# Optimization experiments

Hardware: AMD Instinct MI355X
Metric: run time of the kernel (lower is better)

## Reference

```python
import jax, jax.numpy as jnp
import numpy as np

B, LI, LT, DM, H = 1, 2048, 384, 2560, 20
DH = DM // H  # 128
EPS = 1e-05


def _rms(x, w):
    # torch.nn.RMSNorm over last dim (inner_dim), elementwise affine w
    return x * jax.lax.rsqrt(jnp.mean(x * x, axis=-1, keepdims=True) + EPS) * w


def _apply_rope(x, rope):
    # x: [B, L, H, D]; rope: [1, L, 1, D/2, 2, 2] (flux-style freqs_cis)
    xr = x.reshape(x.shape[0], x.shape[1], x.shape[2], -1, 1, 2)  # [B,L,H,D/2,1,2]
    out = rope[..., 0] * xr[..., 0] + rope[..., 1] * xr[..., 1]   # [B,L,H,D/2,2]
    return out.reshape(x.shape)


def _sdpa(q, k, v):
    # q,k,v: [B, L, H, D] -> out [B, L, H*D]; scale 1/sqrt(D)
    scale = 1.0 / np.sqrt(q.shape[-1]).astype(np.float32)
    scores = jnp.einsum('bqhd,bkhd->bhqk', q, k) * scale
    p = jax.nn.softmax(scores, axis=-1)
    o = jnp.einsum('bhqk,bkhd->bqhd', p, v)
    return o.reshape(o.shape[0], o.shape[1], -1)


def _lin(x, W, b):
    return x @ W.T + b


def _forward(img, txt, rope, img_masks,
             Wq, bq, Wk, bk, Wv, bv, Wo, bo, qn, kn,
             Wq_t, bq_t, Wk_t, bk_t, Wv_t, bv_t, Wo_t, bo_t, qn_t, kn_t):
    bsz = img.shape[0]
    # img stream: proj -> RMSNorm -> head split
    iq = _rms(_lin(img, Wq, bq), qn).reshape(bsz, -1, H, DH)
    ik = _rms(_lin(img, Wk, bk), kn).reshape(bsz, -1, H, DH)
    iv = _lin(img, Wv, bv).reshape(bsz, -1, H, DH)
    ik = ik * img_masks[:, :, None, None]
    # txt stream
    tq = _rms(_lin(txt, Wq_t, bq_t), qn_t).reshape(bsz, -1, H, DH)
    tk = _rms(_lin(txt, Wk_t, bk_t), kn_t).reshape(bsz, -1, H, DH)
    tv = _lin(txt, Wv_t, bv_t).reshape(bsz, -1, H, DH)
    # concat streams, apply rope, attention
    q = jnp.concatenate([iq, tq], axis=1)
    k = jnp.concatenate([ik, tk], axis=1)
    v = jnp.concatenate([iv, tv], axis=1)
    q = _apply_rope(q, rope)
    k = _apply_rope(k, rope)
    attn = _sdpa(q, k, v)  # [B, LI+LT, DM]
    img_attn, txt_attn = attn[:, :LI], attn[:, LI:]
    return _lin(img_attn, Wo, bo), _lin(txt_attn, Wo_t, bo_t)


def setup_inputs() -> dict:
    key = jax.random.key(0)
    ks = jax.random.split(key, 16)
    s = 0.02
    inp = {
        'img': jax.random.normal(ks[0], (B, LI, DM), jnp.float32),
        'txt': jax.random.normal(ks[1], (B, LT, DM), jnp.float32),
        'rope': jax.random.normal(ks[2], (1, LI + LT, 1, DH // 2, 2, 2), jnp.float32),
        'img_masks': jnp.ones((B, LI), jnp.float32),
    }
    wnames = ['Wq', 'Wk', 'Wv', 'Wo', 'Wq_t', 'Wk_t', 'Wv_t', 'Wo_t']
    for i, n in enumerate(wnames):
        inp[n] = jax.random.normal(ks[3 + i], (DM, DM), jnp.float32) * s
        inp['b' + n[1:]] = jnp.zeros((DM,), jnp.float32)
    for i, n in enumerate(['qn', 'kn', 'qn_t', 'kn_t']):
        inp[n] = jax.random.uniform(ks[11 + i], (DM,), jnp.float32, 0.5, 1.5)
    return inp


def reference(img, txt, rope, img_masks,
              Wq, bq, Wk, bk, Wv, bv, Wo, bo, qn, kn,
              Wq_t, bq_t, Wk_t, bk_t, Wv_t, bv_t, Wo_t, bo_t, qn_t, kn_t):
    return _forward(img, txt, rope, img_masks,
                    Wq, bq, Wk, bk, Wv, bv, Wo, bo, qn, kn,
                    Wq_t, bq_t, Wk_t, bk_t, Wv_t, bv_t, Wo_t, bo_t, qn_t, kn_t)
```

## Files before the change

### kernel.cpp

```cpp
#include <hip/hip_runtime.h>
#include <math.h>

#define LI 2048
#define LT 384
#define LSEQ 2432
#define DM 2560
#define NH 20
#define DH 128
#define SCALE 0.08838834764831845f

typedef __bf16 bf16x8 __attribute__((ext_vector_type(8)));
typedef __bf16 bf16x4 __attribute__((ext_vector_type(4)));
typedef __bf16 bf16x2 __attribute__((ext_vector_type(2)));
typedef float f32x4 __attribute__((ext_vector_type(4)));

__device__ __forceinline__ void async_copy16(const void* gsrc, void* lds_uniform) {
    __builtin_amdgcn_global_load_lds(
        (const __attribute__((address_space(1))) unsigned int*)gsrc,
        (__attribute__((address_space(3))) unsigned int*)lds_uniform,
        16, 0, 0);
}


__global__ __launch_bounds__(256) void cvt8_kernel(
    const float* __restrict__ s0, const float* __restrict__ s1,
    const float* __restrict__ s2, const float* __restrict__ s3,
    const float* __restrict__ s4, const float* __restrict__ s5,
    const float* __restrict__ s6, const float* __restrict__ s7,
    __bf16* __restrict__ dst)
{
    const float* srcs[8] = {s0, s1, s2, s3, s4, s5, s6, s7};
    const float* s = srcs[blockIdx.y];
    __bf16* d = dst + (size_t)blockIdx.y * (size_t)DM * DM;
    int i = blockIdx.x * 256 + threadIdx.x;
    const float4* sp = (const float4*)s + (size_t)i * 2;
    float4 a = sp[0], b = sp[1];
    bf16x8 o = {(__bf16)a.x, (__bf16)a.y, (__bf16)a.z, (__bf16)a.w,
                (__bf16)b.x, (__bf16)b.y, (__bf16)b.z, (__bf16)b.w};
    *((bf16x8*)d + i) = o;
}

__global__ __launch_bounds__(256) void cvt_kernel(
    const float* __restrict__ s, __bf16* __restrict__ d, int n8)
{
    int i = blockIdx.x * 256 + threadIdx.x;
    if (i >= n8) return;
    const float4* sp = (const float4*)s + (size_t)i * 2;
    float4 a = sp[0], b = sp[1];
    bf16x8 o = {(__bf16)a.x, (__bf16)a.y, (__bf16)a.z, (__bf16)a.w,
                (__bf16)b.x, (__bf16)b.y, (__bf16)b.z, (__bf16)b.w};
    *((bf16x8*)d + i) = o;
}


__device__ __forceinline__ void gemm_core(
    const __bf16* __restrict__ Ab,
    const __bf16* __restrict__ Bb,
    const float* __restrict__ bias,
    float* __restrict__ Cb,
    __bf16* sA, __bf16* sB)
{
    const int t = threadIdx.x, wave = t >> 6, lane = t & 63;
    const int l15 = lane & 15, quad = lane >> 4;
    const int wm = wave >> 1, wn = wave & 1;

    f32x4 acc[4][4];
#pragma unroll
    for (int i = 0; i < 4; i++)
#pragma unroll
        for (int j = 0; j < 4; j++) acc[i][j] = f32x4{0.f, 0.f, 0.f, 0.f};

    size_t soff[4];
#pragma unroll
    for (int j = 0; j < 4; j++) {
        int c = j * 256 + t;
        int row = c >> 3, u = c & 7;
        soff[j] = (size_t)row * DM + ((u ^ (row & 7)) * 8);
    }

    for (int k0 = 0; k0 < DM; k0 += 64) {
        __syncthreads();
#pragma unroll
        for (int j = 0; j < 4; j++)
            async_copy16(Ab + soff[j] + k0, (char*)sA + (j * 256 + wave * 64) * 16);
#pragma unroll
        for (int j = 0; j < 4; j++)
            async_copy16(Bb + soff[j] + k0, (char*)sB + (j * 256 + wave * 64) * 16);
        __syncthreads();

#pragma unroll
        for (int ks = 0; ks < 2; ks++) {
            bf16x8 af[4], bg[4];
#pragma unroll
            for (int mt = 0; mt < 4; mt++) {
                int r = wm * 64 + mt * 16 + l15;
                af[mt] = *(const bf16x8*)(sA + r * 64 + (((quad + ks * 4) ^ (r & 7)) * 8));
            }
#pragma unroll
            for (int nt = 0; nt < 4; nt++) {
                int r = wn * 64 + nt * 16 + l15;
                bg[nt] = *(const bf16x8*)(sB + r * 64 + (((quad + ks * 4) ^ (r & 7)) * 8));
            }
#pragma unroll
            for (int mt = 0; mt < 4; mt++)
#pragma unroll
                for (int nt = 0; nt < 4; nt++)
                    acc[mt][nt] = __builtin_amdgcn_mfma_f32_16x16x32_bf16(af[mt], bg[nt], acc[mt][nt], 0, 0, 0);
        }
    }

#pragma unroll
    for (int mt = 0; mt < 4; mt++) {
        const int row = wm * 64 + mt * 16 + quad * 4;
#pragma unroll
        for (int nt = 0; nt < 4; nt++) {
            const int col = wn * 64 + nt * 16 + l15;
            const float bv = bias[col];
            float* cp = Cb + (size_t)row * DM + col;
            cp[0]        = acc[mt][nt][0] + bv;
            cp[DM]       = acc[mt][nt][1] + bv;
            cp[2 * DM]   = acc[mt][nt][2] + bv;
            cp[3 * DM]   = acc[mt][nt][3] + bv;
        }
    }
}

__device__ __forceinline__ void qkv_body(
    int nblk, int mblk,
    const __bf16* __restrict__ xbf, const __bf16* __restrict__ wbf,
    const float* __restrict__ bq, const float* __restrict__ bk, const float* __restrict__ bv,
    const float* __restrict__ bq_t, const float* __restrict__ bk_t, const float* __restrict__ bv_t,
    float* __restrict__ qraw, float* __restrict__ kraw, float* __restrict__ vraw,
    __bf16* sA, __bf16* sB)
{
    const int which = nblk / 20;
    const int nloc = (nblk % 20) * 128;
    const bool is_txt = (mblk >= 16);
    const size_t WELEM = (size_t)DM * DM;
    const int widx = which + (is_txt ? 4 : 0);
    const __bf16* W = wbf + (size_t)widx * WELEM;
    const float* bias = (which == 0) ? (is_txt ? bq_t : bq)
                      : (which == 1) ? (is_txt ? bk_t : bk)
                                     : (is_txt ? bv_t : bv);
    float* C = (which == 0) ? qraw : (which == 1) ? kraw : vraw;
    gemm_core(xbf + (size_t)mblk * 128 * DM, W + (size_t)nloc * DM, bias + nloc,
              C + (size_t)mblk * 128 * DM + nloc, sA, sB);
}

__global__ __launch_bounds__(256, 4) void gemm_qkv_a_kernel(
    const __bf16* __restrict__ xbf, const __bf16* __restrict__ wbf,
    const float* __restrict__ bq, const float* __restrict__ bk, const float* __restrict__ bv,
    const float* __restrict__ bq_t, const float* __restrict__ bk_t, const float* __restrict__ bv_t,
    float* __restrict__ qraw, float* __restrict__ kraw, float* __restrict__ vraw)
{
    __shared__ alignas(16) __bf16 sA[128 * 64];
    __shared__ alignas(16) __bf16 sB[128 * 64];
    qkv_body(blockIdx.x, blockIdx.y, xbf, wbf, bq, bk, bv, bq_t, bk_t, bv_t,
             qraw, kraw, vraw, sA, sB);
}

__global__ __launch_bounds__(256, 4) void gemm_qkv_b_kernel(
    const __bf16* __restrict__ xbf, const __bf16* __restrict__ wbf,
    const float* __restrict__ bq, const float* __restrict__ bk, const float* __restrict__ bv,
    const float* __restrict__ bq_t, const float* __restrict__ bk_t, const float* __restrict__ bv_t,
    float* __restrict__ qraw, float* __restrict__ kraw, float* __restrict__ vraw)
{
    __shared__ alignas(16) __bf16 sA[128 * 64];
    __shared__ alignas(16) __bf16 sB[128 * 64];
    qkv_body(blockIdx.x, blockIdx.y + 10, xbf, wbf, bq, bk, bv, bq_t, bk_t, bv_t,
             qraw, kraw, vraw, sA, sB);
}

__global__ __launch_bounds__(256, 4) void gemm_out_kernel(
    const __bf16* __restrict__ attnbf, const __bf16* __restrict__ wbf,
    const float* __restrict__ bo, const float* __restrict__ bo_t,
    float* __restrict__ out)
{
    __shared__ alignas(16) __bf16 sA[128 * 64];
    __shared__ alignas(16) __bf16 sB[128 * 64];
    const int nblk = blockIdx.x, mblk = blockIdx.y;
    const bool is_txt = (mblk >= 16);
    const size_t WELEM = (size_t)DM * DM;
    const __bf16* W = wbf + (size_t)(is_txt ? 7 : 3) * WELEM;
    const float* bias = (is_txt ? bo_t : bo) + nblk * 128;
    gemm_core(attnbf + (size_t)mblk * 128 * DM, W + (size_t)nblk * 128 * DM, bias,
              out + (size_t)mblk * 128 * DM + nblk * 128, sA, sB);
}


__global__ __launch_bounds__(256) void rmsrope_kernel(
    const float* __restrict__ qraw, const float* __restrict__ kraw,
    const float* __restrict__ rope, const float* __restrict__ img_masks,
    const float* __restrict__ qn, const float* __restrict__ kn,
    const float* __restrict__ qn_t, const float* __restrict__ kn_t,
    __bf16* __restrict__ qbf, __bf16* __restrict__ kbf)
{
    const int l = blockIdx.x, t = threadIdx.x;
    const int wave = t >> 6, lane = t & 63;
    const bool is_img = (l < LI);
    const float* qw = is_img ? qn : qn_t;
    const float* kw = is_img ? kn : kn_t;
    const float kmask = is_img ? img_masks[l] : 1.0f;
    const float* qr = qraw + (size_t)l * DM;
    const float* kr = kraw + (size_t)l * DM;

    float2 qv[5], kv[5];
    float sq = 0.f, sk = 0.f;
#pragma unroll
    for (int j = 0; j < 5; j++) {
        int c2 = j * 256 + t;
        qv[j] = *(const float2*)(qr + 2 * c2);
        kv[j] = *(const float2*)(kr + 2 * c2);
        sq += qv[j].x * qv[j].x + qv[j].y * qv[j].y;
        sk += kv[j].x * kv[j].x + kv[j].y * kv[j].y;
    }
#pragma unroll
    for (int m = 32; m; m >>= 1) { sq += __shfl_xor(sq, m); sk += __shfl_xor(sk, m); }
    __shared__ float redq[4], redk[4];
    if (lane == 0) { redq[wave] = sq; redk[wave] = sk; }
    __syncthreads();
    sq = redq[0] + redq[1] + redq[2] + redq[3];
    sk = redk[0] + redk[1] + redk[2] + redk[3];
    const float rq = rsqrtf(sq * (1.0f / DM) + 1e-5f);
    const float rk = rsqrtf(sk * (1.0f / DM) + 1e-5f) * kmask;

#pragma unroll
    for (int j = 0; j < 5; j++) {
        int c2 = j * 256 + t;
        int c = 2 * c2;
        float4 rp = *(const float4*)(rope + ((size_t)l * 64 + (c2 & 63)) * 4);
        float2 w2q = *(const float2*)(qw + c);
        float2 w2k = *(const float2*)(kw + c);
        float x0 = qv[j].x * rq * w2q.x, x1 = qv[j].y * rq * w2q.y;
        bf16x2 oq = {(__bf16)(rp.x * x0 + rp.y * x1), (__bf16)(rp.z * x0 + rp.w * x1)};
        *(bf16x2*)(qbf + (size_t)l * DM + c) = oq;
        float y0 = kv[j].x * rk * w2k.x, y1 = kv[j].y * rk * w2k.y;
        bf16x2 ok = {(__bf16)(rp.x * y0 + rp.y * y1), (__bf16)(rp.z * y0 + rp.w * y1)};
        *(bf16x2*)(kbf + (size_t)l * DM + c) = ok;
    }
}


__global__ __launch_bounds__(256) void transpose_cvt_kernel(
    const float* __restrict__ src, __bf16* __restrict__ dst)
{
    __shared__ float tile[32][33];
    const int c0 = blockIdx.x * 32;
    const int r0 = blockIdx.y * 32;
    const int tc = threadIdx.x & 31, tr = threadIdx.x >> 5;
#pragma unroll
    for (int j = 0; j < 4; j++)
        tile[tr + j * 8][tc] = src[(size_t)(r0 + tr + j * 8) * DM + c0 + tc];
    __syncthreads();
#pragma unroll
    for (int j = 0; j < 4; j++)
        dst[(size_t)(c0 + tr + j * 8) * LSEQ + r0 + tc] = (__bf16)tile[tc][tr + j * 8];
}


__global__ __launch_bounds__(256, 4) void flash_kernel(
    const __bf16* __restrict__ qb, const __bf16* __restrict__ kb,
    const __bf16* __restrict__ vt, __bf16* __restrict__ ob)
{
    __shared__ alignas(16) __bf16 sK[64 * DH];
    __shared__ alignas(16) __bf16 sV[DH * 64];
    __shared__ alignas(16) __bf16 sP[4 * 16 * 64];
    const int head = blockIdx.x;
    const int q0 = blockIdx.y * 64;
    const int t = threadIdx.x, wave = t >> 6, lane = t & 63;
    const int l15 = lane & 15, quad = lane >> 4;
    const int qrow = q0 + wave * 16 + l15;

    bf16x8 aq[4];
#pragma unroll
    for (int d = 0; d < 4; d++)
        aq[d] = *(const bf16x8*)(qb + (size_t)qrow * DM + head * DH + d * 32 + quad * 8);

    int koff[4], voff[4];
#pragma unroll
    for (int j = 0; j < 4; j++) {
        int ck = (wave * 4 + j) * 64 + lane;
        int krow = ck >> 4, ku = (ck & 15) ^ (krow & 7);
        koff[j] = krow * DM + head * DH + ku * 8;
        int cv = (wave * 4 + j) * 64 + lane;
        int vrow = cv >> 3, vu = (cv & 7) ^ (vrow & 7);
        voff[j] = (head * DH + vrow) * LSEQ + vu * 8;
    }
    char* const dK = (char*)sK + wave * 4096 + lane * 16;
    char* const dV = (char*)sV + wave * 4096 + lane * 16;

    f32x4 o[8];
#pragma unroll
    for (int i = 0; i < 8; i++) o[i] = f32x4{0.f, 0.f, 0.f, 0.f};
    float m_i = -INFINITY, l_i = 0.f;
    __bf16* pw = sP + wave * (16 * 64);

    bf16x8 rk[4], rv[4];
#pragma unroll
    for (int j = 0; j < 4; j++) {
        rk[j] = *(const bf16x8*)(kb + koff[j]);
        rv[j] = *(const bf16x8*)(vt + voff[j]);
    }

    for (int kv0 = 0; kv0 < LSEQ; kv0 += 64) {
        __syncthreads();
#pragma unroll
        for (int j = 0; j < 4; j++) {
            *(bf16x8*)(dK + j * 1024) = rk[j];
            *(bf16x8*)(dV + j * 1024) = rv[j];
        }
        __syncthreads();

        if (kv0 + 64 < LSEQ) {
#pragma unroll
            for (int j = 0; j < 4; j++) {
                rk[j] = *(const bf16x8*)(kb + koff[j] + (size_t)(kv0 + 64) * DM);
                rv[j] = *(const bf16x8*)(vt + voff[j] + (kv0 + 64));
            }
        }

        f32x4 st[4];
        __builtin_amdgcn_s_setprio(1);
#pragma unroll
        for (int b = 0; b < 4; b++) {
            st[b] = f32x4{0.f, 0.f, 0.f, 0.f};
#pragma unroll
            for (int d = 0; d < 4; d++) {
                int row = b * 16 + l15;
                bf16x8 ak = *(const bf16x8*)(sK + row * 128 + (((d * 4 + quad) ^ (row & 7)) * 8));
                st[b] = __builtin_amdgcn_mfma_f32_16x16x32_bf16(ak, aq[d], st[b], 0, 0, 0);
            }
        }
        __builtin_amdgcn_s_setprio(0);

        float mx = m_i;
#pragma unroll
        for (int b = 0; b < 4; b++)
#pragma unroll
            for (int r = 0; r < 4; r++) { st[b][r] *= SCALE; mx = fmaxf(mx, st[b][r]); }
        mx = fmaxf(mx, __shfl_xor(mx, 16));
        mx = fmaxf(mx, __shfl_xor(mx, 32));
        const float al = __expf(m_i - mx);
        m_i = mx;
        float sum = 0.f;
#pragma unroll
        for (int b = 0; b < 4; b++)
#pragma unroll
            for (int r = 0; r < 4; r++) {
                float p = __expf(st[b][r] - mx);
                st[b][r] = p;
                sum += p;
            }
        sum += __shfl_xor(sum, 16);
        sum += __shfl_xor(sum, 32);
        l_i = l_i * al + sum;

#pragma unroll
        for (int b = 0; b < 4; b++) {
            bf16x4 pk = {(__bf16)st[b][0], (__bf16)st[b][1], (__bf16)st[b][2], (__bf16)st[b][3]};
            int u = 2 * b + (quad >> 1);
            *(bf16x4*)(pw + l15 * 64 + ((u ^ (l15 & 7)) * 8) + (quad & 1) * 4) = pk;
        }

        float alr[4];
#pragma unroll
        for (int r = 0; r < 4; r++) alr[r] = __shfl(al, quad * 4 + r);
#pragma unroll
        for (int i = 0; i < 8; i++) {
            f32x4 tmp = o[i];
            tmp[0] *= alr[0]; tmp[1] *= alr[1]; tmp[2] *= alr[2]; tmp[3] *= alr[3];
            o[i] = tmp;
        }
        __asm__ volatile("s_waitcnt lgkmcnt(0)" ::: "memory");

        bf16x8 ap0 = *(const bf16x8*)(pw + l15 * 64 + ((quad ^ (l15 & 7)) * 8));
        bf16x8 ap1 = *(const bf16x8*)(pw + l15 * 64 + (((4 + quad) ^ (l15 & 7)) * 8));
        __builtin_amdgcn_s_setprio(1);
#pragma unroll
        for (int n2 = 0; n2 < 8; n2++) {
            int row = n2 * 16 + l15;
            bf16x8 bv0 = *(const bf16x8*)(sV + row * 64 + ((quad ^ (row & 7)) * 8));
            bf16x8 bv1 = *(const bf16x8*)(sV + row * 64 + (((4 + quad) ^ (row & 7)) * 8));
            o[n2] = __builtin_amdgcn_mfma_f32_16x16x32_bf16(ap0, bv0, o[n2], 0, 0, 0);
            o[n2] = __builtin_amdgcn_mfma_f32_16x16x32_bf16(ap1, bv1, o[n2], 0, 0, 0);
        }
        __builtin_amdgcn_s_setprio(0);
    }

    const float inv = 1.0f / l_i;
    float invr[4];
#pragma unroll
    for (int r = 0; r < 4; r++) invr[r] = __shfl(inv, quad * 4 + r);
#pragma unroll
    for (int n2 = 0; n2 < 8; n2++)
#pragma unroll
        for (int r = 0; r < 4; r++)
            ob[(size_t)(q0 + wave * 16 + quad * 4 + r) * DM + head * DH + n2 * 16 + l15] =
                (__bf16)(o[n2][r] * invr[r]);
}


extern "C" void kernel_launch(void* const* d_in, const int* in_sizes, int n_in,
                              void* d_out, int out_size, void* d_ws, size_t ws_size,
                              hipStream_t stream) {
    const float* img       = (const float*)d_in[0];
    const float* txt       = (const float*)d_in[1];
    const float* rope      = (const float*)d_in[2];
    const float* img_masks = (const float*)d_in[3];
    const float* Wq   = (const float*)d_in[4];  const float* bq   = (const float*)d_in[5];
    const float* Wk   = (const float*)d_in[6];  const float* bk   = (const float*)d_in[7];
    const float* Wv   = (const float*)d_in[8];  const float* bv   = (const float*)d_in[9];
    const float* Wo   = (const float*)d_in[10]; const float* bo   = (const float*)d_in[11];
    const float* Wq_t = (const float*)d_in[12]; const float* bq_t = (const float*)d_in[13];
    const float* Wk_t = (const float*)d_in[14]; const float* bk_t = (const float*)d_in[15];
    const float* Wv_t = (const float*)d_in[16]; const float* bv_t = (const float*)d_in[17];
    const float* Wo_t = (const float*)d_in[18]; const float* bo_t = (const float*)d_in[19];
    const float* qn   = (const float*)d_in[20]; const float* kn   = (const float*)d_in[21];
    const float* qn_t = (const float*)d_in[22]; const float* kn_t = (const float*)d_in[23];
    float* out = (float*)d_out;

    const size_t WELEM = (size_t)DM * DM;
    const size_t XELEM = (size_t)LSEQ * DM;

    __bf16* wbf  = (__bf16*)d_ws;
    __bf16* xbf  = wbf + 8 * WELEM;
    float*  qraw = (float*)(xbf + XELEM);
    float*  kraw = qraw + XELEM;
    float*  vraw = kraw + XELEM;
    __bf16* qbf  = (__bf16*)(vraw + XELEM);
    __bf16* kbf  = qbf + XELEM;
    __bf16* vt   = kbf + XELEM;
    __bf16* attnbf = (__bf16*)qraw;

    cvt8_kernel<<<dim3((int)(WELEM / 8 / 256), 8), 256, 0, stream>>>(
        Wq, Wk, Wv, Wo, Wq_t, Wk_t, Wv_t, Wo_t, wbf);
    cvt_kernel<<<dim3((LI * DM / 8 + 255) / 256), 256, 0, stream>>>(img, xbf, LI * DM / 8);
    cvt_kernel<<<dim3((LT * DM / 8 + 255) / 256), 256, 0, stream>>>(
        txt, xbf + (size_t)LI * DM, LT * DM / 8);

    gemm_qkv_a_kernel<<<dim3(60, 10), 256, 0, stream>>>(
        xbf, wbf, bq, bk, bv, bq_t, bk_t, bv_t, qraw, kraw, vraw);
    gemm_qkv_b_kernel<<<dim3(60, 9), 256, 0, stream>>>(
        xbf, wbf, bq, bk, bv, bq_t, bk_t, bv_t, qraw, kraw, vraw);

    rmsrope_kernel<<<dim3(LSEQ), 256, 0, stream>>>(
        qraw, kraw, rope, img_masks, qn, kn, qn_t, kn_t, qbf, kbf);

    transpose_cvt_kernel<<<dim3(DM / 32, LSEQ / 32), 256, 0, stream>>>(vraw, vt);

    flash_kernel<<<dim3(NH, LSEQ / 64), 256, 0, stream>>>(qbf, kbf, vt, attnbf);

    gemm_out_kernel<<<dim3(20, 19), 256, 0, stream>>>(attnbf, wbf, bo, bo_t, out);
}
```

Before: 612.1 us.

## Double-buffer flash attention K/V with async LDS loads and 128-row Q tiles

```diff
diff --git a/kernel.cpp b/kernel.cpp
--- a/kernel.cpp
+++ b/kernel.cpp
@@ -8,6 +8,8 @@
 #define NH 20
 #define DH 128
 #define SCALE 0.08838834764831845f
+#define NKV 38
+#define KVBUF 32768
 
 typedef __bf16 bf16x8 __attribute__((ext_vector_type(8)));
 typedef __bf16 bf16x4 __attribute__((ext_vector_type(4)));
@@ -258,145 +260,167 @@
 }
 
 
-__global__ __launch_bounds__(256, 4) void flash_kernel(
+__global__ __launch_bounds__(256, 2) void flash_kernel(
     const __bf16* __restrict__ qb, const __bf16* __restrict__ kb,
     const __bf16* __restrict__ vt, __bf16* __restrict__ ob)
 {
-    __shared__ alignas(16) __bf16 sK[64 * DH];
-    __shared__ alignas(16) __bf16 sV[DH * 64];
-    __shared__ alignas(16) __bf16 sP[4 * 16 * 64];
+    extern __shared__ __align__(16) char smem[];
     const int head = blockIdx.x;
-    const int q0 = blockIdx.y * 64;
+    const int q0 = blockIdx.y * 128;
     const int t = threadIdx.x, wave = t >> 6, lane = t & 63;
     const int l15 = lane & 15, quad = lane >> 4;
-    const int qrow = q0 + wave * 16 + l15;
-
-    bf16x8 aq[4];
-#pragma unroll
-    for (int d = 0; d < 4; d++)
-        aq[d] = *(const bf16x8*)(qb + (size_t)qrow * DM + head * DH + d * 32 + quad * 8);
+
+    bf16x8 aq[2][4];
+#pragma unroll
+    for (int s = 0; s < 2; s++)
+#pragma unroll
+        for (int d = 0; d < 4; d++)
+            aq[s][d] = *(const bf16x8*)(qb + (size_t)(q0 + wave * 32 + s * 16 + l15) * DM
+                                        + head * DH + d * 32 + quad * 8);
 
     int koff[4], voff[4];
 #pragma unroll
     for (int j = 0; j < 4; j++) {
-        int ck = (wave * 4 + j) * 64 + lane;
-        int krow = ck >> 4, ku = (ck & 15) ^ (krow & 7);
+        int c = j * 256 + t;
+        int krow = c >> 4, ku = (c & 15) ^ (krow & 7);
         koff[j] = krow * DM + head * DH + ku * 8;
-        int cv = (wave * 4 + j) * 64 + lane;
-        int vrow = cv >> 3, vu = (cv & 7) ^ (vrow & 7);
+        int vrow = c >> 3, vu = (c & 7) ^ (vrow & 7);
         voff[j] = (head * DH + vrow) * LSEQ + vu * 8;
     }
-    char* const dK = (char*)sK + wave * 4096 + lane * 16;
-    char* const dV = (char*)sV + wave * 4096 + lane * 16;
-
-    f32x4 o[8];
-#pragma unroll
-    for (int i = 0; i < 8; i++) o[i] = f32x4{0.f, 0.f, 0.f, 0.f};
-    float m_i = -INFINITY, l_i = 0.f;
-    __bf16* pw = sP + wave * (16 * 64);
-
-    bf16x8 rk[4], rv[4];
+    const int dunit = wave * 64 * 16;
+
+    f32x4 o0[8], o1[8];
+#pragma unroll
+    for (int i = 0; i < 8; i++) { o0[i] = f32x4{0.f,0.f,0.f,0.f}; o1[i] = f32x4{0.f,0.f,0.f,0.f}; }
+    float m0 = -INFINITY, m1 = -INFINITY, li0 = 0.f, li1 = 0.f;
+    __bf16* pw0 = (__bf16*)(smem + 2 * KVBUF) + (wave * 2 + 0) * (16 * 64);
+    __bf16* pw1 = (__bf16*)(smem + 2 * KVBUF) + (wave * 2 + 1) * (16 * 64);
+
 #pragma unroll
     for (int j = 0; j < 4; j++) {
-        rk[j] = *(const bf16x8*)(kb + koff[j]);
-        rv[j] = *(const bf16x8*)(vt + voff[j]);
-    }
-
-    for (int kv0 = 0; kv0 < LSEQ; kv0 += 64) {
-        __syncthreads();
-#pragma unroll
-        for (int j = 0; j < 4; j++) {
-            *(bf16x8*)(dK + j * 1024) = rk[j];
-            *(bf16x8*)(dV + j * 1024) = rv[j];
-        }
-        __syncthreads();
-
-        if (kv0 + 64 < LSEQ) {
+        async_copy16(kb + koff[j], smem + j * 4096 + dunit);
+        async_copy16(vt + voff[j], smem + 16384 + j * 4096 + dunit);
+    }
+
+    for (int it = 0; it < NKV; ++it) {
+        const int kv0 = it * 64;
+        char* cur = smem + (it & 1) * KVBUF;
+        char* nxt = smem + ((it + 1) & 1) * KVBUF;
+        if (it + 1 < NKV) {
 #pragma unroll
             for (int j = 0; j < 4; j++) {
-                rk[j] = *(const bf16x8*)(kb + koff[j] + (size_t)(kv0 + 64) * DM);
-                rv[j] = *(const bf16x8*)(vt + voff[j] + (kv0 + 64));
-            }
-        }
-
-        f32x4 st[4];
+                async_copy16(kb + koff[j] + (size_t)(kv0 + 64) * DM, nxt + j * 4096 + dunit);
+                async_copy16(vt + voff[j] + (kv0 + 64), nxt + 16384 + j * 4096 + dunit);
+            }
+            asm volatile("s_waitcnt vmcnt(8)" ::: "memory");
+        } else {
+            asm volatile("s_waitcnt vmcnt(0)" ::: "memory");
+        }
+        __builtin_amdgcn_s_barrier();
+        __builtin_amdgcn_sched_barrier(0);
+        const __bf16* sK = (const __bf16*)cur;
+        const __bf16* sV = (const __bf16*)(cur + 16384);
+
+        f32x4 st0[4], st1[4];
         __builtin_amdgcn_s_setprio(1);
 #pragma unroll
         for (int b = 0; b < 4; b++) {
-            st[b] = f32x4{0.f, 0.f, 0.f, 0.f};
+            st0[b] = f32x4{0.f,0.f,0.f,0.f};
+            st1[b] = f32x4{0.f,0.f,0.f,0.f};
 #pragma unroll
             for (int d = 0; d < 4; d++) {
                 int row = b * 16 + l15;
                 bf16x8 ak = *(const bf16x8*)(sK + row * 128 + (((d * 4 + quad) ^ (row & 7)) * 8));
-                st[b] = __builtin_amdgcn_mfma_f32_16x16x32_bf16(ak, aq[d], st[b], 0, 0, 0);
+                st0[b] = __builtin_amdgcn_mfma_f32_16x16x32_bf16(ak, aq[0][d], st0[b], 0, 0, 0);
+                st1[b] = __builtin_amdgcn_mfma_f32_16x16x32_bf16(ak, aq[1][d], st1[b], 0, 0, 0);
             }
         }
         __builtin_amdgcn_s_setprio(0);
 
-        float mx = m_i;
+        float mx0 = m0, mx1 = m1;
 #pragma unroll
         for (int b = 0; b < 4; b++)
 #pragma unroll
-            for (int r = 0; r < 4; r++) { st[b][r] *= SCALE; mx = fmaxf(mx, st[b][r]); }
-        mx = fmaxf(mx, __shfl_xor(mx, 16));
-        mx = fmaxf(mx, __shfl_xor(mx, 32));
-        const float al = __expf(m_i - mx);
-        m_i = mx;
-        float sum = 0.f;
+            for (int r = 0; r < 4; r++) {
+                st0[b][r] *= SCALE; mx0 = fmaxf(mx0, st0[b][r]);
+                st1[b][r] *= SCALE; mx1 = fmaxf(mx1, st1[b][r]);
+            }
+        mx0 = fmaxf(mx0, __shfl_xor(mx0, 16)); mx0 = fmaxf(mx0, __shfl_xor(mx0, 32));
+        mx1 = fmaxf(mx1, __shfl_xor(mx1, 16)); mx1 = fmaxf(mx1, __shfl_xor(mx1, 32));
+        const float al0 = __expf(m0 - mx0); m0 = mx0;
+        const float al1 = __expf(m1 - mx1); m1 = mx1;
+        float sum0 = 0.f, sum1 = 0.f;
 #pragma unroll
         for (int b = 0; b < 4; b++)
 #pragma unroll
             for (int r = 0; r < 4; r++) {
-                float p = __expf(st[b][r] - mx);
-                st[b][r] = p;
-                sum += p;
-            }
-        sum += __shfl_xor(sum, 16);
-        sum += __shfl_xor(sum, 32);
-        l_i = l_i * al + sum;
+                float p0 = __expf(st0[b][r] - mx0); st0[b][r] = p0; sum0 += p0;
+                float p1 = __expf(st1[b][r] - mx1); st1[b][r] = p1; sum1 += p1;
+            }
+        sum0 += __shfl_xor(sum0, 16); sum0 += __shfl_xor(sum0, 32);
+        sum1 += __shfl_xor(sum1, 16); sum1 += __shfl_xor(sum1, 32);
+        li0 = li0 * al0 + sum0;
+        li1 = li1 * al1 + sum1;
 
 #pragma unroll
         for (int b = 0; b < 4; b++) {
-            bf16x4 pk = {(__bf16)st[b][0], (__bf16)st[b][1], (__bf16)st[b][2], (__bf16)st[b][3]};
             int u = 2 * b + (quad >> 1);
-            *(bf16x4*)(pw + l15 * 64 + ((u ^ (l15 & 7)) * 8) + (quad & 1) * 4) = pk;
-        }
-
-        float alr[4];
-#pragma unroll
-        for (int r = 0; r < 4; r++) alr[r] = __shfl(al, quad * 4 + r);
+            bf16x4 pk0 = {(__bf16)st0[b][0], (__bf16)st0[b][1], (__bf16)st0[b][2], (__bf16)st0[b][3]};
+            *(bf16x4*)(pw0 + l15 * 64 + ((u ^ (l15 & 7)) * 8) + (quad & 1) * 4) = pk0;
+            bf16x4 pk1 = {(__bf16)st1[b][0], (__bf16)st1[b][1], (__bf16)st1[b][2], (__bf16)st1[b][3]};
+            *(bf16x4*)(pw1 + l15 * 64 + ((u ^ (l15 & 7)) * 8) + (quad & 1) * 4) = pk1;
+        }
+
+        float alr0[4], alr1[4];
+#pragma unroll
+        for (int r = 0; r < 4; r++) {
+            alr0[r] = __shfl(al0, quad * 4 + r);
+            alr1[r] = __shfl(al1, quad * 4 + r);
+        }
 #pragma unroll
         for (int i = 0; i < 8; i++) {
-            f32x4 tmp = o[i];
-            tmp[0] *= alr[0]; tmp[1] *= alr[1]; tmp[2] *= alr[2]; tmp[3] *= alr[3];
-            o[i] = tmp;
+            f32x4 t0 = o0[i], t1 = o1[i];
+            t0[0] *= alr0[0]; t0[1] *= alr0[1]; t0[2] *= alr0[2]; t0[3] *= alr0[3];
+            t1[0] *= alr1[0]; t1[1] *= alr1[1]; t1[2] *= alr1[2]; t1[3] *= alr1[3];
+            o0[i] = t0; o1[i] = t1;
         }
         __asm__ volatile("s_waitcnt lgkmcnt(0)" ::: "memory");
 
-        bf16x8 ap0 = *(const bf16x8*)(pw + l15 * 64 + ((quad ^ (l15 & 7)) * 8));
-        bf16x8 ap1 = *(const bf16x8*)(pw + l15 * 64 + (((4 + quad) ^ (l15 & 7)) * 8));
+        bf16x8 ap00 = *(const bf16x8*)(pw0 + l15 * 64 + ((quad ^ (l15 & 7)) * 8));
+        bf16x8 ap01 = *(const bf16x8*)(pw0 + l15 * 64 + (((4 + quad) ^ (l15 & 7)) * 8));
+        bf16x8 ap10 = *(const bf16x8*)(pw1 + l15 * 64 + ((quad ^ (l15 & 7)) * 8));
+        bf16x8 ap11 = *(const bf16x8*)(pw1 + l15 * 64 + (((4 + quad) ^ (l15 & 7)) * 8));
         __builtin_amdgcn_s_setprio(1);
 #pragma unroll
         for (int n2 = 0; n2 < 8; n2++) {
             int row = n2 * 16 + l15;
             bf16x8 bv0 = *(const bf16x8*)(sV + row * 64 + ((quad ^ (row & 7)) * 8));
             bf16x8 bv1 = *(const bf16x8*)(sV + row * 64 + (((4 + quad) ^ (row & 7)) * 8));
-            o[n2] = __builtin_amdgcn_mfma_f32_16x16x32_bf16(ap0, bv0, o[n2], 0, 0, 0);
-            o[n2] = __builtin_amdgcn_mfma_f32_16x16x32_bf16(ap1, bv1, o[n2], 0, 0, 0);
+            o0[n2] = __builtin_amdgcn_mfma_f32_16x16x32_bf16(ap00, bv0, o0[n2], 0, 0, 0);
+            o0[n2] = __builtin_amdgcn_mfma_f32_16x16x32_bf16(ap01, bv1, o0[n2], 0, 0, 0);
+            o1[n2] = __builtin_amdgcn_mfma_f32_16x16x32_bf16(ap10, bv0, o1[n2], 0, 0, 0);
+            o1[n2] = __builtin_amdgcn_mfma_f32_16x16x32_bf16(ap11, bv1, o1[n2], 0, 0, 0);
         }
         __builtin_amdgcn_s_setprio(0);
-    }
-
-    const float inv = 1.0f / l_i;
-    float invr[4];
-#pragma unroll
-    for (int r = 0; r < 4; r++) invr[r] = __shfl(inv, quad * 4 + r);
+        __builtin_amdgcn_s_barrier();
+    }
+
+    const float inv0 = 1.0f / li0, inv1 = 1.0f / li1;
+    float ivr0[4], ivr1[4];
+#pragma unroll
+    for (int r = 0; r < 4; r++) {
+        ivr0[r] = __shfl(inv0, quad * 4 + r);
+        ivr1[r] = __shfl(inv1, quad * 4 + r);
+    }
 #pragma unroll
     for (int n2 = 0; n2 < 8; n2++)
 #pragma unroll
-        for (int r = 0; r < 4; r++)
-            ob[(size_t)(q0 + wave * 16 + quad * 4 + r) * DM + head * DH + n2 * 16 + l15] =
-                (__bf16)(o[n2][r] * invr[r]);
+        for (int r = 0; r < 4; r++) {
+            ob[(size_t)(q0 + wave * 32 + quad * 4 + r) * DM + head * DH + n2 * 16 + l15] =
+                (__bf16)(o0[n2][r] * ivr0[r]);
+            ob[(size_t)(q0 + wave * 32 + 16 + quad * 4 + r) * DM + head * DH + n2 * 16 + l15] =
+                (__bf16)(o1[n2][r] * ivr1[r]);
+        }
 }
 
 
@@ -419,6 +443,13 @@
     const float* qn_t = (const float*)d_in[22]; const float* kn_t = (const float*)d_in[23];
     float* out = (float*)d_out;
 
+    static bool inited = false;
+    if (!inited) {
+        hipFuncSetAttribute(reinterpret_cast<const void*>(flash_kernel),
+                            hipFuncAttributeMaxDynamicSharedMemorySize, 81920);
+        inited = true;
+    }
+
     const size_t WELEM = (size_t)DM * DM;
     const size_t XELEM = (size_t)LSEQ * DM;
 
@@ -448,7 +479,7 @@
 
     transpose_cvt_kernel<<<dim3(DM / 32, LSEQ / 32), 256, 0, stream>>>(vraw, vt);
 
-    flash_kernel<<<dim3(NH, LSEQ / 64), 256, 0, stream>>>(qbf, kbf, vt, attnbf);
+    flash_kernel<<<dim3(NH, LSEQ / 128), 256, 81920, stream>>>(qbf, kbf, vt, attnbf);
 
     gemm_out_kernel<<<dim3(20, 19), 256, 0, stream>>>(attnbf, wbf, bo, bo_t, out);
 }
```

After: 600.1 us. About the same (-2.0%).

## Restructure flash attention with 32x32 MFMA, split-KV waves and async LDS loads

Applied to the files above, without the earlier changes.

```diff
diff --git a/kernel.cpp b/kernel.cpp
--- a/kernel.cpp
+++ b/kernel.cpp
@@ -8,11 +8,13 @@
 #define NH 20
 #define DH 128
 #define SCALE 0.08838834764831845f
+#define NKV 38
 
 typedef __bf16 bf16x8 __attribute__((ext_vector_type(8)));
 typedef __bf16 bf16x4 __attribute__((ext_vector_type(4)));
 typedef __bf16 bf16x2 __attribute__((ext_vector_type(2)));
 typedef float f32x4 __attribute__((ext_vector_type(4)));
+typedef float f32x16 __attribute__((ext_vector_type(16)));
 
 __device__ __forceinline__ void async_copy16(const void* gsrc, void* lds_uniform) {
     __builtin_amdgcn_global_load_lds(
@@ -258,145 +260,161 @@
 }
 
 
-__global__ __launch_bounds__(256, 4) void flash_kernel(
+__global__ __launch_bounds__(256, 3) void flash_kernel(
     const __bf16* __restrict__ qb, const __bf16* __restrict__ kb,
     const __bf16* __restrict__ vt, __bf16* __restrict__ ob)
 {
-    __shared__ alignas(16) __bf16 sK[64 * DH];
-    __shared__ alignas(16) __bf16 sV[DH * 64];
-    __shared__ alignas(16) __bf16 sP[4 * 16 * 64];
+    __shared__ alignas(16) char smem[34816];
     const int head = blockIdx.x;
     const int q0 = blockIdx.y * 64;
     const int t = threadIdx.x, wave = t >> 6, lane = t & 63;
-    const int l15 = lane & 15, quad = lane >> 4;
-    const int qrow = q0 + wave * 16 + l15;
-
-    bf16x8 aq[4];
-#pragma unroll
-    for (int d = 0; d < 4; d++)
-        aq[d] = *(const bf16x8*)(qb + (size_t)qrow * DM + head * DH + d * 32 + quad * 8);
+    const int s = wave >> 1, h = wave & 1;
+    const int l31 = lane & 31, h5 = lane >> 5;
+
+    bf16x8 bq8[8];
+    {
+        const __bf16* qp = qb + (size_t)(q0 + s * 32 + l31) * DM + head * DH;
+#pragma unroll
+        for (int t8 = 0; t8 < 8; t8++)
+            bq8[t8] = *(const bf16x8*)(qp + t8 * 16 + h5 * 8);
+    }
 
     int koff[4], voff[4];
 #pragma unroll
     for (int j = 0; j < 4; j++) {
-        int ck = (wave * 4 + j) * 64 + lane;
-        int krow = ck >> 4, ku = (ck & 15) ^ (krow & 7);
+        int c = j * 256 + t;
+        int krow = c >> 4, ku = (c & 15) ^ (krow & 7);
         koff[j] = krow * DM + head * DH + ku * 8;
-        int cv = (wave * 4 + j) * 64 + lane;
-        int vrow = cv >> 3, vu = (cv & 7) ^ (vrow & 7);
+        int vrow = c >> 3, vu = (c & 7) ^ (vrow & 7);
         voff[j] = (head * DH + vrow) * LSEQ + vu * 8;
     }
-    char* const dK = (char*)sK + wave * 4096 + lane * 16;
-    char* const dV = (char*)sV + wave * 4096 + lane * 16;
-
-    f32x4 o[8];
-#pragma unroll
-    for (int i = 0; i < 8; i++) o[i] = f32x4{0.f, 0.f, 0.f, 0.f};
+    const int dunit = wave * 1024;
+
+    const __bf16* sK = (const __bf16*)smem;
+    const __bf16* sV = (const __bf16*)(smem + 16384);
+    const int kbase = 32 * h;
+
+    f32x16 o[4];
+#pragma unroll
+    for (int dt = 0; dt < 4; dt++)
+#pragma unroll
+        for (int e = 0; e < 16; e++) o[dt][e] = 0.f;
     float m_i = -INFINITY, l_i = 0.f;
-    __bf16* pw = sP + wave * (16 * 64);
-
-    bf16x8 rk[4], rv[4];
-#pragma unroll
-    for (int j = 0; j < 4; j++) {
-        rk[j] = *(const bf16x8*)(kb + koff[j]);
-        rv[j] = *(const bf16x8*)(vt + voff[j]);
-    }
-
-    for (int kv0 = 0; kv0 < LSEQ; kv0 += 64) {
+
+    for (int it = 0; it < NKV; ++it) {
         __syncthreads();
 #pragma unroll
         for (int j = 0; j < 4; j++) {
-            *(bf16x8*)(dK + j * 1024) = rk[j];
-            *(bf16x8*)(dV + j * 1024) = rv[j];
+            async_copy16(kb + koff[j] + (size_t)(it * 64) * DM, smem + j * 4096 + dunit);
+            async_copy16(vt + voff[j] + it * 64, smem + 16384 + j * 4096 + dunit);
         }
         __syncthreads();
 
-        if (kv0 + 64 < LSEQ) {
-#pragma unroll
-            for (int j = 0; j < 4; j++) {
-                rk[j] = *(const bf16x8*)(kb + koff[j] + (size_t)(kv0 + 64) * DM);
-                rv[j] = *(const bf16x8*)(vt + voff[j] + (kv0 + 64));
-            }
-        }
-
-        f32x4 st[4];
+        f32x16 st;
+#pragma unroll
+        for (int e = 0; e < 16; e++) st[e] = 0.f;
         __builtin_amdgcn_s_setprio(1);
 #pragma unroll
-        for (int b = 0; b < 4; b++) {
-            st[b] = f32x4{0.f, 0.f, 0.f, 0.f};
-#pragma unroll
-            for (int d = 0; d < 4; d++) {
-                int row = b * 16 + l15;
-                bf16x8 ak = *(const bf16x8*)(sK + row * 128 + (((d * 4 + quad) ^ (row & 7)) * 8));
-                st[b] = __builtin_amdgcn_mfma_f32_16x16x32_bf16(ak, aq[d], st[b], 0, 0, 0);
-            }
+        for (int t8 = 0; t8 < 8; t8++) {
+            int row = kbase + l31;
+            int unit = (2 * t8 + h5) ^ (row & 7);
+            bf16x8 ak = *(const bf16x8*)(sK + row * 128 + unit * 8);
+            st = __builtin_amdgcn_mfma_f32_32x32x16_bf16(ak, bq8[t8], st, 0, 0, 0);
         }
         __builtin_amdgcn_s_setprio(0);
 
         float mx = m_i;
 #pragma unroll
-        for (int b = 0; b < 4; b++)
-#pragma unroll
-            for (int r = 0; r < 4; r++) { st[b][r] *= SCALE; mx = fmaxf(mx, st[b][r]); }
-        mx = fmaxf(mx, __shfl_xor(mx, 16));
+        for (int e = 0; e < 16; e++) { st[e] *= SCALE; mx = fmaxf(mx, st[e]); }
         mx = fmaxf(mx, __shfl_xor(mx, 32));
         const float al = __expf(m_i - mx);
         m_i = mx;
         float sum = 0.f;
 #pragma unroll
-        for (int b = 0; b < 4; b++)
-#pragma unroll
-            for (int r = 0; r < 4; r++) {
-                float p = __expf(st[b][r] - mx);
-                st[b][r] = p;
-                sum += p;
-            }
-        sum += __shfl_xor(sum, 16);
+        for (int e = 0; e < 16; e++) { float p = __expf(st[e] - mx); st[e] = p; sum += p; }
         sum += __shfl_xor(sum, 32);
         l_i = l_i * al + sum;
-
-#pragma unroll
-        for (int b = 0; b < 4; b++) {
-            bf16x4 pk = {(__bf16)st[b][0], (__bf16)st[b][1], (__bf16)st[b][2], (__bf16)st[b][3]};
-            int u = 2 * b + (quad >> 1);
-            *(bf16x4*)(pw + l15 * 64 + ((u ^ (l15 & 7)) * 8) + (quad & 1) * 4) = pk;
-        }
-
-        float alr[4];
-#pragma unroll
-        for (int r = 0; r < 4; r++) alr[r] = __shfl(al, quad * 4 + r);
-#pragma unroll
-        for (int i = 0; i < 8; i++) {
-            f32x4 tmp = o[i];
-            tmp[0] *= alr[0]; tmp[1] *= alr[1]; tmp[2] *= alr[2]; tmp[3] *= alr[3];
-            o[i] = tmp;
-        }
-        __asm__ volatile("s_waitcnt lgkmcnt(0)" ::: "memory");
-
-        bf16x8 ap0 = *(const bf16x8*)(pw + l15 * 64 + ((quad ^ (l15 & 7)) * 8));
-        bf16x8 ap1 = *(const bf16x8*)(pw + l15 * 64 + (((4 + quad) ^ (l15 & 7)) * 8));
+#pragma unroll
+        for (int dt = 0; dt < 4; dt++)
+#pragma unroll
+            for (int e = 0; e < 16; e++) o[dt][e] *= al;
+
+        bf16x8 pfrag[2];
+#pragma unroll
+        for (int c = 0; c < 2; c++) {
+            union { bf16x2 v; unsigned u; } A, B, C, D;
+            A.v = bf16x2{(__bf16)st[8 * c + 0], (__bf16)st[8 * c + 1]};
+            B.v = bf16x2{(__bf16)st[8 * c + 2], (__bf16)st[8 * c + 3]};
+            C.v = bf16x2{(__bf16)st[8 * c + 4], (__bf16)st[8 * c + 5]};
+            D.v = bf16x2{(__bf16)st[8 * c + 6], (__bf16)st[8 * c + 7]};
+            unsigned xA = __shfl_xor(A.u, 32), xB = __shfl_xor(B.u, 32);
+            unsigned xC = __shfl_xor(C.u, 32), xD = __shfl_xor(D.u, 32);
+            union { unsigned w[4]; bf16x8 v; } pf;
+            pf.w[0] = h5 ? xC : A.u;
+            pf.w[1] = h5 ? xD : B.u;
+            pf.w[2] = h5 ? C.u : xA;
+            pf.w[3] = h5 ? D.u : xB;
+            pfrag[c] = pf.v;
+        }
+
         __builtin_amdgcn_s_setprio(1);
 #pragma unroll
-        for (int n2 = 0; n2 < 8; n2++) {
-            int row = n2 * 16 + l15;
-            bf16x8 bv0 = *(const bf16x8*)(sV + row * 64 + ((quad ^ (row & 7)) * 8));
-            bf16x8 bv1 = *(const bf16x8*)(sV + row * 64 + (((4 + quad) ^ (row & 7)) * 8));
-            o[n2] = __builtin_amdgcn_mfma_f32_16x16x32_bf16(ap0, bv0, o[n2], 0, 0, 0);
-            o[n2] = __builtin_amdgcn_mfma_f32_16x16x32_bf16(ap1, bv1, o[n2], 0, 0, 0);
+        for (int dt = 0; dt < 4; dt++) {
+            int row = dt * 32 + l31;
+#pragma unroll
+            for (int c = 0; c < 2; c++) {
+                int unit = (4 * h + 2 * c + h5) ^ (row & 7);
+                bf16x8 av = *(const bf16x8*)(sV + row * 64 + unit * 8);
+                o[dt] = __builtin_amdgcn_mfma_f32_32x32x16_bf16(av, pfrag[c], o[dt], 0, 0, 0);
+            }
         }
         __builtin_amdgcn_s_setprio(0);
     }
 
-    const float inv = 1.0f / l_i;
-    float invr[4];
-#pragma unroll
-    for (int r = 0; r < 4; r++) invr[r] = __shfl(inv, quad * 4 + r);
-#pragma unroll
-    for (int n2 = 0; n2 < 8; n2++)
-#pragma unroll
-        for (int r = 0; r < 4; r++)
-            ob[(size_t)(q0 + wave * 16 + quad * 4 + r) * DM + head * DH + n2 * 16 + l15] =
-                (__bf16)(o[n2][r] * invr[r]);
+    __syncthreads();
+    float* mlbuf = (float*)(smem + 33792);
+    if (lane < 32) {
+        mlbuf[((s * 2 + h) * 2 + 0) * 32 + lane] = m_i;
+        mlbuf[((s * 2 + h) * 2 + 1) * 32 + lane] = l_i;
+    }
+    __syncthreads();
+    const float pm = mlbuf[((s * 2 + (h ^ 1)) * 2 + 0) * 32 + l31];
+    const float pl = mlbuf[((s * 2 + (h ^ 1)) * 2 + 1) * 32 + l31];
+    const float M = fmaxf(m_i, pm);
+    const float sc = __expf(m_i - M), psc = __expf(pm - M);
+    const float L = l_i * sc + pl * psc;
+    const float fac = sc / L;
+    float* obuf = (float*)smem + s * 4224;
+    if (h == 1) {
+#pragma unroll
+        for (int dt = 0; dt < 4; dt++)
+#pragma unroll
+            for (int e = 0; e < 16; e++) {
+                int dout = dt * 32 + (e & 3) + 8 * (e >> 2) + 4 * h5;
+                obuf[l31 * 132 + dout] = o[dt][e] * fac;
+            }
+    }
+    __syncthreads();
+    if (h == 0) {
+#pragma unroll
+        for (int dt = 0; dt < 4; dt++)
+#pragma unroll
+            for (int e = 0; e < 16; e++) {
+                int dout = dt * 32 + (e & 3) + 8 * (e >> 2) + 4 * h5;
+                int idx = l31 * 132 + dout;
+                obuf[idx] = o[dt][e] * fac + obuf[idx];
+            }
+    }
+    __syncthreads();
+#pragma unroll
+    for (int rr = 0; rr < 8; rr++) {
+        int qblk = wave * 16 + h5 * 8 + rr;
+        int ss = qblk >> 5, qq = qblk & 31;
+        const float* src = (const float*)smem + ss * 4224 + qq * 132 + l31 * 4;
+        float4 v4 = *(const float4*)src;
+        bf16x4 ov = {(__bf16)v4.x, (__bf16)v4.y, (__bf16)v4.z, (__bf16)v4.w};
+        *(bf16x4*)(ob + (size_t)(q0 + qblk) * DM + head * DH + l31 * 4) = ov;
+    }
 }
 
 
```

Measured after the change: 583.7 us. -4.6%, faster.
